# Kernel tuning notes

Measured on AMD Instinct MI355X. Metric: run time of the kernel, lower is better.

## Reference

```python
import jax, jax.numpy as jnp
import numpy as np

D = 64      # node_input_dim == node_hidden_dim
EIN = 16    # edge_input_dim
EH = 64     # edge_hidden_dim
NL, NR = 5000, 15000
EL, ER = 50000, 150000
STEPS = 6
EPS = 1e-5
SLOPE = 0.01


def _ln(x, g, b):
    mu = jnp.mean(x, axis=-1, keepdims=True)
    v = jnp.mean((x - mu) ** 2, axis=-1, keepdims=True)
    return (x - mu) / jnp.sqrt(v + EPS) * g + b


def _lrelu(x):
    return jnp.where(x > 0, x, SLOPE * x)


def setup_inputs() -> dict:
    key = jax.random.key(0)
    ks = jax.random.split(key, 32)

    def n(k, shape, fan_in):
        return jax.random.normal(k, shape, jnp.float32) * (fan_in ** -0.5)

    return {
        'lig_n_feat': jax.random.normal(ks[0], (NL, D), jnp.float32),
        'lig_e_feat': jax.random.normal(ks[1], (EL, EIN), jnp.float32),
        'lig_src': jax.random.randint(ks[2], (EL,), 0, NL),
        'lig_dst': jax.random.randint(ks[3], (EL,), 0, NL),
        'rec_n_feat': jax.random.normal(ks[4], (NR, D), jnp.float32),
        'rec_e_feat': jax.random.normal(ks[5], (ER, EIN), jnp.float32),
        'rec_src': jax.random.randint(ks[6], (ER,), 0, NR),
        'rec_dst': jax.random.randint(ks[7], (ER,), 0, NR),
        'mask': jax.random.uniform(ks[8], (NL, NR), jnp.float32),
        # linear0
        'W0': n(ks[9], (D, D), D), 'b0': jnp.zeros((D,), jnp.float32),
        # edge network: Linear(EIN,EH) -> ReLU -> Linear(EH, D*D)
        'We1': n(ks[10], (EH, EIN), EIN), 'be1': jnp.zeros((EH,), jnp.float32),
        'We2': n(ks[11], (D * D, EH), EH), 'be2': jnp.zeros((D * D,), jnp.float32),
        # NNConv residual fc (no bias) and conv bias
        'resW': n(ks[12], (D, D), D), 'conv_b': jnp.zeros((D,), jnp.float32),
        # message layer Linear(2D, D)
        'msgW': n(ks[13], (D, 2 * D), 2 * D), 'msgb': jnp.zeros((D,), jnp.float32),
        # attention projections (no bias)
        'Qlig': n(ks[14], (D, D), D), 'Klig': n(ks[15], (D, D), D), 'Vlig': n(ks[16], (D, D), D),
        'Qrec': n(ks[17], (D, D), D), 'Krec': n(ks[18], (D, D), D), 'Vrec': n(ks[19], (D, D), D),
        # final LayerNorms
        'g_lig': jnp.ones((D,), jnp.float32), 'b_lig': jnp.zeros((D,), jnp.float32),
        'g_rec': jnp.ones((D,), jnp.float32), 'b_rec': jnp.zeros((D,), jnp.float32),
    }


def _gather_branch(x, efeat, src, dst, n_nodes, W0, b0, We1, be1, We2, be2, resW, conv_b, msgW, msgb):
    # per-edge weight matrices from edge MLP: [E, D, D] (in x out)
    We = jax.nn.relu(efeat @ We1.T + be1) @ We2.T + be2
    We = We.reshape(-1, D, D)
    h = jax.nn.relu(x @ W0.T + b0)
    for _ in range(STEPS):
        msg = jnp.einsum('ei,eio->eo', h[src], We)          # gather + per-edge transform
        agg = jax.ops.segment_sum(msg, dst, num_segments=n_nodes)  # scatter-sum
        m = jax.nn.relu(agg + h @ resW.T + conv_b)           # NNConv residual + bias, relu
        h = jnp.concatenate([m, h], axis=1) @ msgW.T + msgb  # message_layer
    return h + x


def reference(lig_n_feat, lig_e_feat, lig_src, lig_dst, rec_n_feat, rec_e_feat, rec_src, rec_dst,
              mask, W0, b0, We1, be1, We2, be2, resW, conv_b, msgW, msgb,
              Qlig, Klig, Vlig, Qrec, Krec, Vrec, g_lig, b_lig, g_rec, b_rec):
    lig_Fv = _gather_branch(lig_n_feat, lig_e_feat, lig_src, lig_dst, NL,
                            W0, b0, We1, be1, We2, be2, resW, conv_b, msgW, msgb)
    rec_Fv = _gather_branch(rec_n_feat, rec_e_feat, rec_src, rec_dst, NR,
                            W0, b0, We1, be1, We2, be2, resW, conv_b, msgW, msgb)
    hl = _ln(lig_Fv, g_lig, b_lig)
    hr = _ln(rec_Fv, g_rec, b_rec)
    # lig attends to rec
    ql, kr, vr = _lrelu(hl @ Qlig.T), _lrelu(hr @ Krec.T), hr @ Vrec.T
    a = mask * (ql @ kr.T) - 1000.0 * (1.0 - mask)
    att_lig = jax.nn.softmax(a, axis=1) @ vr
    # rec attends to lig
    qr, kl, vl = _lrelu(hr @ Qrec.T), _lrelu(hl @ Klig.T), hl @ Vlig.T
    mt = mask.T
    a2 = mt * (qr @ kl.T) - 1000.0 * (1.0 - mt)
    att_rec = jax.nn.softmax(a2, axis=1) @ vl
    return (_ln(att_lig, g_lig, b_lig), _ln(att_rec, g_rec, b_rec))
```

## Files before the change

### kernel.cpp

```cpp
#include <hip/hip_runtime.h>
#include <hip/hip_bf16.h>

typedef unsigned short ushort_t;
typedef __attribute__((ext_vector_type(8))) short short8_t;
typedef __attribute__((ext_vector_type(4))) float f32x4;
typedef __attribute__((ext_vector_type(4))) unsigned uint4_t;

#define NLIG 5000
#define NREC 15000
#define NTOT 20000
#define ELIG 50000
#define EREC 150000
#define ETOT 200000
#define VSTRIDE 20160
#define NB0 313
#define NB1 938

__device__ __forceinline__ float us2f(ushort_t u){
  union { float f; unsigned int i; } x; x.i = ((unsigned int)u) << 16; return x.f;
}
__device__ __forceinline__ ushort_t f2us(float f){
  __hip_bfloat16 b = __float2bfloat16(f);
  return *reinterpret_cast<ushort_t*>(&b);
}
__device__ __forceinline__ unsigned pkbf(float a, float b){
  return (unsigned)f2us(a) | ((unsigned)f2us(b) << 16);
}
__device__ __forceinline__ float wsum64(float v){
#pragma unroll
  for (int s = 32; s >= 1; s >>= 1) v += __shfl_xor(v, s, 64);
  return v;
}
__device__ __forceinline__ f32x4 mfma32(short8_t a, short8_t b, f32x4 c){
  return __builtin_amdgcn_mfma_f32_16x16x32_bf16(a, b, c, 0, 0, 0);
}
__device__ __forceinline__ int geti(const int* __restrict__ p, int i, int i64){
  return i64 ? p[2*i] : p[i];
}

__global__ void kdetect2(const unsigned* __restrict__ xw, const unsigned* __restrict__ iw,
                         int* __restrict__ flagp){
  const int lane = threadIdx.x;
  unsigned w = xw[lane];
  int e0 = (int)((w >> 7) & 0xFF);
  int hit = (e0 >= 100 && e0 <= 134) ? 1 : 0;
  int zodd = ((lane & 1) && iw[lane] == 0u) ? 1 : 0;
#pragma unroll
  for (int s = 32; s >= 1; s >>= 1){
    hit  += __shfl_xor(hit,  s, 64);
    zodd += __shfl_xor(zodd, s, 64);
  }
  if (lane == 0){
    flagp[0] = (hit  >= 40) ? 1 : 0;
    flagp[1] = (zodd >= 24) ? 1 : 0;
  }
}

__global__ void ksent(float* __restrict__ out, int n, float c){
  int i = blockIdx.x*256 + threadIdx.x;
  if (i < n) out[i] = c;
}

__global__ void kcvt_x(const void* __restrict__ lx, const void* __restrict__ rx,
                       const int* __restrict__ flagp, float* __restrict__ xall){
  const int flag = flagp[0];
  const int idx = blockIdx.x*256 + threadIdx.x;
  const void* src; int local;
  if (idx < NLIG*64){ src = lx; local = idx; } else { src = rx; local = idx - NLIG*64; }
  float v;
  if (flag) v = us2f(((const ushort_t*)src)[local]);
  else      v = ((const float*)src)[local];
  xall[idx] = v;
}

struct Srcs { const void* p[20]; };
__global__ void kcvt_w(Srcs S, const int* __restrict__ flagp, float* __restrict__ wcvt){
  const int bounds[21] = {0,4096,4160,5184,5248,267392,271488,275584,275648,283840,
                          283904,288000,292096,296192,300288,304384,308480,308544,308608,308672,308736};
  const int flag = flagp[0];
  const int idx = blockIdx.x*256 + threadIdx.x;
  if (idx >= 308736) return;
  int seg = 0;
#pragma unroll
  for (int s = 1; s < 20; ++s) if (idx >= bounds[s]) seg = s;
  const void* src = S.p[0];
#pragma unroll
  for (int s = 1; s < 20; ++s) if (seg == s) src = S.p[s];
  const int local = idx - bounds[seg];
  float v;
  if (flag) v = us2f(((const ushort_t*)src)[local]);
  else      v = ((const float*)src)[local];
  wcvt[idx] = v;
}

#define W_W0    0
#define W_B0    4096
#define W_WE1   4160
#define W_BE1   5184
#define W_WE2   5248
#define W_BE2   267392
#define W_RESW  271488
#define W_CONVB 275584
#define W_MSGW  275648
#define W_MSGB  283840
#define W_QLIG  283904
#define W_KLIG  288000
#define W_VLIG  292096
#define W_QREC  296192
#define W_KREC  300288
#define W_VREC  304384
#define W_GLIG  308480
#define W_BLIG  308544
#define W_GREC  308608
#define W_BREC  308672

__global__ void kWpk(const float* __restrict__ We2f, ushort_t* __restrict__ Wpk){
  int oidx = blockIdx.x*256 + threadIdx.x;
  int j = oidx & 7, lane = (oidx >> 3) & 63, p = (oidx >> 9) & 1;
  int t = (oidx >> 10) & 3, kb = oidx >> 12;
  int o = t*16 + (lane & 15);
  int gik = kb*32 + (lane >> 4)*8 + j;
  int i = gik >> 6, k = gik & 63;
  float v = We2f[(size_t)(i*64 + o)*64 + k];
  ushort_t hi = f2us(v);
  Wpk[oidx] = p ? f2us(v - us2f(hi)) : hi;
}

__global__ void kh0(const float* __restrict__ xall, const float* __restrict__ W0f,
                    const float* __restrict__ b0f, float* __restrict__ h){
  __shared__ float xr[4][64];
  const int lane = threadIdx.x & 63, wv = threadIdx.x >> 6;
  const int n = blockIdx.x*4 + wv;
  xr[wv][lane] = xall[(size_t)n*64 + lane];
  __syncthreads();
  float acc = b0f[lane];
  const float* wr = W0f + lane*64;
#pragma unroll
  for (int i = 0; i < 64; ++i) acc += xr[wv][i] * wr[i];
  h[(size_t)n*64 + lane] = acc > 0.f ? acc : 0.f;
}

__global__ void khist(const int* __restrict__ ldst, const int* __restrict__ rdst,
                      const int* __restrict__ flagp, int* __restrict__ counts){
  const int i64 = flagp[1];
  const int e = blockIdx.x*256 + threadIdx.x;
  if (e >= ETOT) return;
  int dstg = (e < ELIG) ? geti(ldst, e, i64) : geti(rdst, e - ELIG, i64) + NLIG;
  atomicAdd(&counts[dstg], 1);
}

__global__ __launch_bounds__(1024) void kscan(const int* __restrict__ counts, int* __restrict__ offs){
  __shared__ int part[1024];
  const int tid = threadIdx.x;
  const int PER = 20;
  int loc[PER]; int s = 0;
#pragma unroll
  for (int j = 0; j < PER; ++j){ int idx = tid*PER + j; int v = (idx < NTOT) ? counts[idx] : 0; loc[j] = s; s += v; }
  part[tid] = s;
  __syncthreads();
  for (int d = 1; d < 1024; d <<= 1){
    int add = (tid >= d) ? part[tid - d] : 0;
    __syncthreads();
    part[tid] += add;
    __syncthreads();
  }
  int pre = (tid > 0) ? part[tid - 1] : 0;
#pragma unroll
  for (int j = 0; j < PER; ++j){ int idx = tid*PER + j; if (idx < NTOT) offs[idx] = pre + loc[j]; }
  if (tid == 1023) offs[NTOT] = part[1023];
}

__global__ void kfill(const int* __restrict__ lsrc, const int* __restrict__ ldst,
                      const int* __restrict__ rsrc, const int* __restrict__ rdst,
                      const void* __restrict__ lef, const void* __restrict__ ref_,
                      const int* __restrict__ offs, int* __restrict__ cursor,
                      const int* __restrict__ flagp,
                      int* __restrict__ e_srcn, float* __restrict__ ef_srt){
  const int flag = flagp[0];
  const int i64  = flagp[1];
  const int e = blockIdx.x*256 + threadIdx.x;
  if (e >= ETOT) return;
  int srcg, dstg, le; const void* efb;
  if (e < ELIG){ srcg = geti(lsrc, e, i64); dstg = geti(ldst, e, i64); efb = lef; le = e; }
  else {
    int e2 = e - ELIG;
    srcg = geti(rsrc, e2, i64) + NLIG; dstg = geti(rdst, e2, i64) + NLIG; efb = ref_; le = e2;
  }
  int pos = offs[dstg] + atomicAdd(&cursor[dstg], 1);
  e_srcn[pos] = srcg;
  float* efd = ef_srt + (size_t)pos*16;
  if (flag){
    const ushort_t* efp = (const ushort_t*)efb + (size_t)le*16;
#pragma unroll
    for (int c = 0; c < 16; ++c) efd[c] = us2f(efp[c]);
  } else {
    const float* efp = (const float*)efb + (size_t)le*16;
#pragma unroll
    for (int c = 0; c < 16; ++c) efd[c] = efp[c];
  }
}

__global__ __launch_bounds__(1024)
void kstep(const float* __restrict__ hin, float* __restrict__ hout,
           const int* __restrict__ offs, const int* __restrict__ e_srcn,
           const float* __restrict__ ef_srt,
           const ushort_t* __restrict__ Wpk,
           const float* __restrict__ We1f, const float* __restrict__ be1f,
           const float* __restrict__ resWf, const float* __restrict__ convbf,
           const float* __restrict__ msgWf, const float* __restrict__ msgbf,
           const float* __restrict__ be2f){
  __shared__ alignas(16) char sbuf[65536];
  __shared__ float h_lds[1024];
  __shared__ float Hs_lds[1024];
  __shared__ float m_lds[1024];
  __shared__ float cbf[64], mbf[64];

  const int tid = threadIdx.x, lane = tid & 63, wv = tid >> 6;
  const int n0 = blockIdx.x * 16;

  h_lds[tid] = hin[(size_t)n0*64 + tid];
  if (tid < 64){ cbf[tid] = convbf[tid]; mbf[tid] = msgbf[tid]; }

  float w1r[16];
#pragma unroll
  for (int c = 0; c < 16; ++c) w1r[c] = We1f[lane*16 + c];
  const float b1 = be1f[lane];

  float sacc[64];
#pragma unroll
  for (int i = 0; i < 64; ++i) sacc[i] = 0.f;
  float hs = 0.f;
  {
    const int v = n0 + wv;
    const int jb = offs[v], je = offs[v+1];
    for (int j = jb; j < je; ++j){
      const int sn = e_srcn[j];
      const float* efp = ef_srt + (size_t)j*16;
      float zl = b1;
#pragma unroll
      for (int c = 0; c < 16; ++c) zl += efp[c] * w1r[c];
      zl = zl > 0.f ? zl : 0.f;
      hs += hin[(size_t)sn*64 + lane];
      const float4* hp = (const float4*)(hin + (size_t)sn*64);
#pragma unroll
      for (int i4 = 0; i4 < 16; ++i4){
        float4 hv = hp[i4];
        sacc[i4*4+0] += hv.x * zl;
        sacc[i4*4+1] += hv.y * zl;
        sacc[i4*4+2] += hv.z * zl;
        sacc[i4*4+3] += hv.w * zl;
      }
    }
    Hs_lds[wv*64 + lane] = hs;
  }

  const int r15 = lane & 15, g4 = lane >> 4;
  const int tW = wv & 3, kq = wv >> 2;
  f32x4 acc; acc[0]=0.f; acc[1]=0.f; acc[2]=0.f; acc[3]=0.f;
  const unsigned sswz = ((unsigned)(wv & 7)) << 4;
  const unsigned rswz = ((unsigned)(r15 & 7)) << 4;
#pragma unroll
  for (int c = 0; c < 4; ++c){
#pragma unroll
    for (int ii = 0; ii < 16; ++ii){
      float v = sacc[c*16 + ii];
      ushort_t hi16 = f2us(v);
      unsigned off = ((unsigned)(wv*2048 + (ii*64 + lane)*2)) ^ sswz;
      *(ushort_t*)(sbuf + off) = hi16;
      *(ushort_t*)(sbuf + 32768 + off) = f2us(v - us2f(hi16));
    }
    __syncthreads();
    for (int kk = 0; kk < 8; ++kk){
      const int lk = kq*256 + kk*32;
      const int kb = c*32 + kq*8 + kk;
      const unsigned aoff = ((unsigned)(r15*2048 + (lk + g4*8)*2)) ^ rswz;
      const short8_t ah = *(const short8_t*)(sbuf + aoff);
      const short8_t al = *(const short8_t*)(sbuf + 32768 + aoff);
      const ushort_t* bp = Wpk + (size_t)(kb*4 + tW)*1024 + lane*8;
      const short8_t bh = *(const short8_t*)(bp);
      const short8_t bl = *(const short8_t*)(bp + 512);
      acc = mfma32(ah, bh, acc);
      acc = mfma32(ah, bl, acc);
      acc = mfma32(al, bh, acc);
    }
    __syncthreads();
  }

  float* redf  = (float*)sbuf;
  float* be2s  = (float*)(sbuf + 16384);
  float* resWt = (float*)(sbuf + 32768);
#pragma unroll
  for (int q = 0; q < 4; ++q)
    redf[kq*1024 + (g4*4 + q)*64 + tW*16 + r15] = acc[q];
  for (int idx = tid; idx < 4096; idx += 1024){
    be2s[idx] = be2f[idx];
    resWt[(idx & 63)*65 + (idx >> 6)] = resWf[idx];
  }
  __syncthreads();
  {
    float aggv = cbf[lane];
#pragma unroll
    for (int k4 = 0; k4 < 4; ++k4) aggv += redf[k4*1024 + wv*64 + lane];
    float t1 = 0.f, t2 = 0.f;
#pragma unroll 8
    for (int i = 0; i < 64; ++i){
      t1 += Hs_lds[wv*64 + i] * be2s[i*64 + lane];
      t2 += h_lds[wv*64 + i]  * resWt[i*65 + lane];
    }
    float mv = aggv + t1 + t2;
    m_lds[wv*64 + lane] = mv > 0.f ? mv : 0.f;
  }
  __syncthreads();
  float* msgWt = (float*)sbuf;
  for (int idx = tid; idx < 8192; idx += 1024)
    msgWt[(idx & 127)*65 + (idx >> 7)] = msgWf[idx];
  __syncthreads();
  {
    float hn = mbf[lane];
#pragma unroll 8
    for (int i = 0; i < 64; ++i){
      hn += m_lds[wv*64 + i] * msgWt[i*65 + lane];
      hn += h_lds[wv*64 + i] * msgWt[(64 + i)*65 + lane];
    }
    hout[(size_t)(n0 + wv)*64 + lane] = hn;
  }
}

__global__ void kfvproj(const float* __restrict__ h, const float* __restrict__ xall,
    const float* __restrict__ wcvt,
    ushort_t* __restrict__ qbh, ushort_t* __restrict__ qbl,
    ushort_t* __restrict__ kbh, ushort_t* __restrict__ kbl,
    ushort_t* __restrict__ vbT){
  __shared__ float hr[4][64];
  const int lane = threadIdx.x & 63, wv = threadIdx.x >> 6;
  const int n = blockIdx.x*4 + wv;
  const bool isLig = n < NLIG;
  const float fv = h[(size_t)n*64 + lane] + xall[(size_t)n*64 + lane];
  const float mu = wsum64(fv) * (1.f/64.f);
  const float dd = fv - mu;
  const float var = wsum64(dd*dd) * (1.f/64.f);
  const float gg = wcvt[(isLig ? W_GLIG : W_GREC) + lane];
  const float bb = wcvt[(isLig ? W_BLIG : W_BREC) + lane];
  const float hl = dd * rsqrtf(var + 1e-5f) * gg + bb;
  hr[wv][lane] = hl;
  __syncthreads();
  const float* Qw = wcvt + (isLig ? W_QLIG : W_QREC) + lane*64;
  const float* Kw = wcvt + (isLig ? W_KLIG : W_KREC) + lane*64;
  const float* Vw = wcvt + (isLig ? W_VLIG : W_VREC) + lane*64;
  float qa = 0.f, ka = 0.f, va = 0.f;
#pragma unroll
  for (int i = 0; i < 64; ++i){
    const float hv = hr[wv][i];
    qa += hv * Qw[i];
    ka += hv * Kw[i];
    va += hv * Vw[i];
  }
  qa = qa > 0.f ? qa : 0.01f*qa;
  ka = ka > 0.f ? ka : 0.01f*ka;
  const size_t o = (size_t)n*64 + lane;
  ushort_t qh = f2us(qa); qbh[o] = qh; qbl[o] = f2us(qa - us2f(qh));
  ushort_t kh = f2us(ka); kbh[o] = kh; kbl[o] = f2us(ka - us2f(kh));
  vbT[(size_t)lane*VSTRIDE + n] = f2us(va);
}

__global__ __launch_bounds__(512)
void kattn2(const ushort_t* __restrict__ qbh, const ushort_t* __restrict__ qbl,
            const ushort_t* __restrict__ kbh, const ushort_t* __restrict__ kbl,
            const ushort_t* __restrict__ vbT, const void* __restrict__ maskp,
            const int* __restrict__ flagp, const float* __restrict__ wcvt,
            float* __restrict__ out){
  __shared__ alignas(16) char abuf[34816];
  __shared__ float mred[8][16], lred[8][16];
  float (*m_tile)[16][257] = (float(*)[16][257])abuf;
  float (*ored)[64][17]    = (float(*)[64][17])abuf;

  const int flag = flagp[0];
  const int bx = blockIdx.x;
  const int dirn = (bx < NB0) ? 0 : 1;
  const int bid  = dirn ? (bx - NB0) : bx;
  const int R   = dirn ? NREC : NLIG;
  const int C   = dirn ? NLIG : NREC;
  const int RNB = dirn ? NLIG : 0;
  const int CNB = dirn ? 0 : NLIG;
  const float* gwf = wcvt + (dirn ? W_GREC : W_GLIG);
  const float* bwf = wcvt + (dirn ? W_BREC : W_BLIG);
  float* outp = out + (size_t)RNB*64;

  const int tid = threadIdx.x, lane = tid & 63, wv = tid >> 6;
  const int r15 = lane & 15, g4 = lane >> 4;
  const int rbase = bid * 16;
  int rn = rbase + r15; if (rn > R-1) rn = R-1;

  const ushort_t* qph = qbh + (size_t)(RNB + rn)*64;
  const ushort_t* qpl = qbl + (size_t)(RNB + rn)*64;
  const short8_t qh0a = *(const short8_t*)(qph + g4*8);
  const short8_t qh0b = *(const short8_t*)(qph + 32 + g4*8);
  const short8_t ql0a = *(const short8_t*)(qpl + g4*8);
  const short8_t ql0b = *(const short8_t*)(qpl + 32 + g4*8);

  const int srcA = (((g4 & 1) * 2)     << 4) + r15;
  const int srcB = (((g4 & 1) * 2 + 1) << 4) + r15;
  const bool hiBank = (g4 >> 1) != 0;

  const int s_row = tid >> 5, s_l31 = tid & 31;
  const int s_cl = tid >> 1, s_half = tid & 1;

  float mr[8];
  auto load_tile = [&](int tb2){
    if (dirn == 0){
      int r = rbase + s_row; if (r > R-1) r = R-1;
      const size_t base = (size_t)r*NREC + tb2;
      const int cmax = C-1 - tb2;
      if (flag){
        const ushort_t* mp = (const ushort_t*)maskp + base;
#pragma unroll
        for (int j = 0; j < 8; ++j){
          int cj = s_l31 + 32*j; if (cj > cmax) cj = cmax;
          mr[j] = us2f(mp[cj]);
        }
      } else {
        const float* mp = (const float*)maskp + base;
#pragma unroll
        for (int j = 0; j < 8; ++j){
          int cj = s_l31 + 32*j; if (cj > cmax) cj = cmax;
          mr[j] = mp[cj];
        }
      }
    } else {
      int c = tb2 + s_cl; if (c > C-1) c = C-1;
      int r0 = rbase + s_half*8; if (r0 > R-8) r0 = R-8;
      const size_t base = (size_t)c*NREC + r0;
      if (flag){
        const ushort_t* mp = (const ushort_t*)maskp + base;
        const short8_t v8 = *(const short8_t*)mp;
#pragma unroll
        for (int j = 0; j < 8; ++j) mr[j] = us2f((ushort_t)v8[j]);
      } else {
        const float* mp = (const float*)maskp + base;
        const float4 v0 = *(const float4*)mp;
        const float4 v1 = *(const float4*)(mp + 4);
        mr[0]=v0.x; mr[1]=v0.y; mr[2]=v0.z; mr[3]=v0.w;
        mr[4]=v1.x; mr[5]=v1.y; mr[6]=v1.z; mr[7]=v1.w;
      }
    }
  };

  float mrun = -1e30f, lrun = 0.f;
  f32x4 oacc[4];
#pragma unroll
  for (int t = 0; t < 4; ++t){ oacc[t][0]=0.f; oacc[t][1]=0.f; oacc[t][2]=0.f; oacc[t][3]=0.f; }

  load_tile(0);
  int buf = 0;
  for (int tb = 0; tb < C; tb += 256){
    if (dirn == 0){
#pragma unroll
      for (int j = 0; j < 8; ++j) m_tile[buf][s_row][s_l31 + 32*j] = mr[j];
    } else {
#pragma unroll
      for (int j = 0; j < 8; ++j) m_tile[buf][s_half*8 + j][s_cl] = mr[j];
    }
    if (tb + 256 < C) load_tile(tb + 256);
    __syncthreads();

    const int cb = tb + wv*32;
    int cn0 = cb + r15;      if (cn0 > C-1) cn0 = C-1;
    int cn1 = cb + 16 + r15; if (cn1 > C-1) cn1 = C-1;
    const ushort_t* kp0h = kbh + (size_t)(CNB + cn0)*64;
    const ushort_t* kp0l = kbl + (size_t)(CNB + cn0)*64;
    const ushort_t* kp1h = kbh + (size_t)(CNB + cn1)*64;
    const ushort_t* kp1l = kbl + (size_t)(CNB + cn1)*64;
    f32x4 st0; st0[0]=0.f; st0[1]=0.f; st0[2]=0.f; st0[3]=0.f;
    f32x4 st1 = st0;
    {
      short8_t ka_ = *(const short8_t*)(kp0h + g4*8);
      short8_t kb_ = *(const short8_t*)(kp0h + 32 + g4*8);
      st0 = mfma32(ka_, qh0a, st0); st0 = mfma32(kb_, qh0b, st0);
      st0 = mfma32(ka_, ql0a, st0); st0 = mfma32(kb_, ql0b, st0);
      short8_t kc_ = *(const short8_t*)(kp0l + g4*8);
      short8_t kd_ = *(const short8_t*)(kp0l + 32 + g4*8);
      st0 = mfma32(kc_, qh0a, st0); st0 = mfma32(kd_, qh0b, st0);
    }
    {
      short8_t ka_ = *(const short8_t*)(kp1h + g4*8);
      short8_t kb_ = *(const short8_t*)(kp1h + 32 + g4*8);
      st1 = mfma32(ka_, qh0a, st1); st1 = mfma32(kb_, qh0b, st1);
      st1 = mfma32(ka_, ql0a, st1); st1 = mfma32(kb_, ql0b, st1);
      short8_t kc_ = *(const short8_t*)(kp1l + g4*8);
      short8_t kd_ = *(const short8_t*)(kp1l + 32 + g4*8);
      st1 = mfma32(kc_, qh0a, st1); st1 = mfma32(kd_, qh0b, st1);
    }
    float sv0[4], sv1[4]; float tmax = -1e30f;
#pragma unroll
    for (int j = 0; j < 4; ++j){
      const int c0 = cb + g4*4 + j, c1 = cb + 16 + g4*4 + j;
      const float mv0 = m_tile[buf][r15][wv*32 + g4*4 + j];
      const float mv1 = m_tile[buf][r15][wv*32 + 16 + g4*4 + j];
      sv0[j] = (c0 < C) ? mv0 * (st0[j] + 1000.f) : -1e30f;
      sv1[j] = (c1 < C) ? mv1 * (st1[j] + 1000.f) : -1e30f;
      tmax = fmaxf(tmax, fmaxf(sv0[j], sv1[j]));
    }
    tmax = fmaxf(tmax, __shfl_xor(tmax, 16, 64));
    tmax = fmaxf(tmax, __shfl_xor(tmax, 32, 64));
    const float mnew = fmaxf(mrun, tmax);
    const float corr = __expf(mrun - mnew);
    float ps0[4], ps1[4], psum = 0.f;
#pragma unroll
    for (int j = 0; j < 4; ++j){
      ps0[j] = __expf(sv0[j] - mnew); psum += ps0[j];
      ps1[j] = __expf(sv1[j] - mnew); psum += ps1[j];
    }
    psum += __shfl_xor(psum, 16, 64);
    psum += __shfl_xor(psum, 32, 64);
    lrun = lrun * corr + psum;
    mrun = mnew;
    const unsigned pk0 = pkbf(ps0[0], ps0[1]);
    const unsigned pk1 = pkbf(ps0[2], ps0[3]);
    const unsigned pk2 = pkbf(ps1[0], ps1[1]);
    const unsigned pk3 = pkbf(ps1[2], ps1[3]);
    const unsigned a0 = (unsigned)__shfl((int)pk0, srcA, 64);
    const unsigned a2 = (unsigned)__shfl((int)pk2, srcA, 64);
    const unsigned a1 = (unsigned)__shfl((int)pk1, srcA, 64);
    const unsigned a3 = (unsigned)__shfl((int)pk3, srcA, 64);
    const unsigned b0 = (unsigned)__shfl((int)pk0, srcB, 64);
    const unsigned b2 = (unsigned)__shfl((int)pk2, srcB, 64);
    const unsigned b1 = (unsigned)__shfl((int)pk1, srcB, 64);
    const unsigned b3 = (unsigned)__shfl((int)pk3, srcB, 64);
    uint4_t pw;
    pw[0] = hiBank ? a2 : a0;
    pw[1] = hiBank ? a3 : a1;
    pw[2] = hiBank ? b2 : b0;
    pw[3] = hiBank ? b3 : b1;
    const short8_t pf8 = *reinterpret_cast<const short8_t*>(&pw);
    const ushort_t* vtb = vbT + (size_t)(CNB + cb + g4*8);
#pragma unroll
    for (int t = 0; t < 4; ++t){
#pragma unroll
      for (int q = 0; q < 4; ++q) oacc[t][q] *= corr;
      const short8_t af = *(const short8_t*)(vtb + (size_t)(t*16 + r15)*VSTRIDE);
      oacc[t] = mfma32(af, pf8, oacc[t]);
    }
    buf ^= 1;
  }

  __syncthreads();
  if (g4 == 0){ mred[wv][r15] = mrun; lred[wv][r15] = lrun; }
#pragma unroll
  for (int t = 0; t < 4; ++t)
#pragma unroll
    for (int q = 0; q < 4; ++q)
      ored[wv][t*16 + g4*4 + q][r15] = oacc[t][q];
  __syncthreads();

  for (int rr = 2*wv; rr <= 2*wv + 1; ++rr){
    float mstar = -1e30f;
#pragma unroll
    for (int w = 0; w < 8; ++w) mstar = fmaxf(mstar, mred[w][rr]);
    float lstar = 0.f, ov = 0.f;
#pragma unroll
    for (int w = 0; w < 8; ++w){
      const float e = __expf(mred[w][rr] - mstar);
      lstar += lred[w][rr] * e;
      ov    += ored[w][lane][rr] * e;
    }
    const float att = ov / lstar;
    const float mu = wsum64(att) * (1.f/64.f);
    const float dd = att - mu;
    const float var = wsum64(dd*dd) * (1.f/64.f);
    const float y = dd * rsqrtf(var + 1e-5f) * gwf[lane] + bwf[lane];
    const int rg = rbase + rr;
    if (rg < R) outp[(size_t)rg*64 + lane] = y;
  }
}

extern "C" void kernel_launch(void* const* d_in, const int* in_sizes, int n_in,
                              void* d_out, int out_size, void* d_ws, size_t ws_size,
                              hipStream_t stream){
  const int expsz[29] = {320000,800000,50000,50000,960000,2400000,150000,150000,75000000,
                         4096,64,1024,64,262144,4096,4096,64,8192,64,
                         4096,4096,4096,4096,4096,4096,64,64,64,64};
  bool ok = (n_in == 29);
  if (ok) for (int i = 0; i < 29; ++i) if (in_sizes[i] != expsz[i]) ok = false;
  if (!ok){
    ksent<<<(out_size + 255)/256, 256, 0, stream>>>((float*)d_out, out_size, 10.0f);
    return;
  }

  const void* lig_n = d_in[0];
  const void* lig_e = d_in[1];
  const int* lig_src = (const int*)d_in[2];
  const int* lig_dst = (const int*)d_in[3];
  const void* rec_n = d_in[4];
  const void* rec_e = d_in[5];
  const int* rec_src = (const int*)d_in[6];
  const int* rec_dst = (const int*)d_in[7];
  const void* mask = d_in[8];

  char* p = (char*)d_ws;
  auto carve = [&](size_t bytes)->char*{ char* r = p; p += (bytes + 255) & ~(size_t)255; return r; };
  float*    xall  = (float*)   carve((size_t)NTOT*64*4);
  float*    wcvt  = (float*)   carve((size_t)308736*4);
  float*    h_a   = (float*)   carve((size_t)NTOT*64*4);
  float*    h_b   = (float*)   carve((size_t)NTOT*64*4);
  ushort_t* Wpk   = (ushort_t*)carve((size_t)524288*2);
  ushort_t* qbh   = (ushort_t*)carve((size_t)NTOT*64*2);
  ushort_t* qbl   = (ushort_t*)carve((size_t)NTOT*64*2);
  ushort_t* kbh   = (ushort_t*)carve((size_t)NTOT*64*2);
  ushort_t* kbl   = (ushort_t*)carve((size_t)NTOT*64*2);
  ushort_t* vbT   = (ushort_t*)carve((size_t)64*VSTRIDE*2);
  int*      flag  = (int*)     carve(256);
  int*      counts= (int*)     carve((size_t)2*NTOT*4);
  int*      cursor= counts + NTOT;
  int*      offs  = (int*)     carve((size_t)(NTOT+1)*4);
  int*      e_srcn= (int*)     carve((size_t)ETOT*4);
  float*    ef_srt= (float*)   carve((size_t)ETOT*16*4);

  if ((size_t)(p - (char*)d_ws) > ws_size){
    ksent<<<(out_size + 255)/256, 256, 0, stream>>>((float*)d_out, out_size, 20.0f);
    return;
  }

  Srcs S;
  for (int i = 0; i < 20; ++i) S.p[i] = d_in[9 + i];

  hipMemsetAsync(counts, 0, (size_t)2*NTOT*4, stream);
  hipMemsetAsync(vbT, 0, (size_t)64*VSTRIDE*2, stream);
  kdetect2<<<1, 64, 0, stream>>>((const unsigned*)lig_n, (const unsigned*)lig_src, flag);
  kcvt_x<<<NTOT*64/256, 256, 0, stream>>>(lig_n, rec_n, flag, xall);
  kcvt_w<<<(308736 + 255)/256, 256, 0, stream>>>(S, flag, wcvt);
  kWpk<<<2048, 256, 0, stream>>>(wcvt + W_WE2, Wpk);
  kh0<<<NTOT/4, 256, 0, stream>>>(xall, wcvt + W_W0, wcvt + W_B0, h_a);
  khist<<<(ETOT + 255)/256, 256, 0, stream>>>(lig_dst, rec_dst, flag, counts);
  kscan<<<1, 1024, 0, stream>>>(counts, offs);
  kfill<<<(ETOT + 255)/256, 256, 0, stream>>>(lig_src, lig_dst, rec_src, rec_dst,
                                              lig_e, rec_e, offs, cursor, flag, e_srcn, ef_srt);
  float* hi = h_a; float* ho = h_b;
  for (int s = 0; s < 6; ++s){
    kstep<<<NTOT/16, 1024, 0, stream>>>(hi, ho, offs, e_srcn, ef_srt, Wpk,
                                        wcvt + W_WE1, wcvt + W_BE1, wcvt + W_RESW,
                                        wcvt + W_CONVB, wcvt + W_MSGW, wcvt + W_MSGB,
                                        wcvt + W_BE2);
    float* t = hi; hi = ho; ho = t;
  }
  kfvproj<<<NTOT/4, 256, 0, stream>>>(hi, xall, wcvt, qbh, qbl, kbh, kbl, vbT);
  kattn2<<<NB0 + NB1, 512, 0, stream>>>(qbh, qbl, kbh, kbl, vbT, mask, flag, wcvt,
                                        (float*)d_out);
}
```

Baseline: 2.135 ms.

## Widen attention mask tiles to 512 columns with two-deep register prefetch

The attention kernel now stages 512-column mask tiles per iteration instead of 256. Each wave processes two 32-column sub-blocks per tile, and two register buffers hold prefetched tiles two iterations ahead. The transposed-direction mask load has each thread read 16 contiguous row values for one column, replacing the earlier half-split scheme. The step kernel's LDS split-bf16 staging also swaps its XOR swizzle for a padded row stride. The aim is fewer barriers and better hiding of mask load latency, at the cost of more registers, which may reduce occupancy, and a larger LDS footprint (about 64KB).

New measurement: 2.248 ms. +5.3%, slower.

```diff
diff --git a/kernel.cpp b/kernel.cpp
--- a/kernel.cpp
+++ b/kernel.cpp
@@ -200,6 +200,8 @@
   }
 }
 
+#define SROW 2080
+#define SLO  (16*SROW)
 __global__ __launch_bounds__(1024)
 void kstep(const float* __restrict__ hin, float* __restrict__ hout,
            const int* __restrict__ offs, const int* __restrict__ e_srcn,
@@ -209,7 +211,7 @@
            const float* __restrict__ resWf, const float* __restrict__ convbf,
            const float* __restrict__ msgWf, const float* __restrict__ msgbf,
            const float* __restrict__ be2f){
-  __shared__ alignas(16) char sbuf[65536];
+  __shared__ alignas(16) char sbuf[2*SLO];
   __shared__ float h_lds[1024];
   __shared__ float Hs_lds[1024];
   __shared__ float m_lds[1024];
@@ -257,25 +259,23 @@
   const int r15 = lane & 15, g4 = lane >> 4;
   const int tW = wv & 3, kq = wv >> 2;
   f32x4 acc; acc[0]=0.f; acc[1]=0.f; acc[2]=0.f; acc[3]=0.f;
-  const unsigned sswz = ((unsigned)(wv & 7)) << 4;
-  const unsigned rswz = ((unsigned)(r15 & 7)) << 4;
 #pragma unroll
   for (int c = 0; c < 4; ++c){
 #pragma unroll
     for (int ii = 0; ii < 16; ++ii){
       float v = sacc[c*16 + ii];
       ushort_t hi16 = f2us(v);
-      unsigned off = ((unsigned)(wv*2048 + (ii*64 + lane)*2)) ^ sswz;
+      unsigned off = (unsigned)(wv*SROW + (ii*64 + lane)*2);
       *(ushort_t*)(sbuf + off) = hi16;
-      *(ushort_t*)(sbuf + 32768 + off) = f2us(v - us2f(hi16));
+      *(ushort_t*)(sbuf + SLO + off) = f2us(v - us2f(hi16));
     }
     __syncthreads();
     for (int kk = 0; kk < 8; ++kk){
       const int lk = kq*256 + kk*32;
       const int kb = c*32 + kq*8 + kk;
-      const unsigned aoff = ((unsigned)(r15*2048 + (lk + g4*8)*2)) ^ rswz;
+      const unsigned aoff = (unsigned)(r15*SROW + (lk + g4*8)*2);
       const short8_t ah = *(const short8_t*)(sbuf + aoff);
-      const short8_t al = *(const short8_t*)(sbuf + 32768 + aoff);
+      const short8_t al = *(const short8_t*)(sbuf + SLO + aoff);
       const ushort_t* bp = Wpk + (size_t)(kb*4 + tW)*1024 + lane*8;
       const short8_t bh = *(const short8_t*)(bp);
       const short8_t bl = *(const short8_t*)(bp + 512);
@@ -369,9 +369,9 @@
             const ushort_t* __restrict__ vbT, const void* __restrict__ maskp,
             const int* __restrict__ flagp, const float* __restrict__ wcvt,
             float* __restrict__ out){
-  __shared__ alignas(16) char abuf[34816];
+  __shared__ alignas(16) char abuf[65664];
   __shared__ float mred[8][16], lred[8][16];
-  float (*m_tile)[16][257] = (float(*)[16][257])abuf;
+  float (*m_tile)[16][513] = (float(*)[16][513])abuf;
   float (*ored)[64][17]    = (float(*)[64][17])abuf;
 
   const int flag = flagp[0];
@@ -403,10 +403,13 @@
   const bool hiBank = (g4 >> 1) != 0;
 
   const int s_row = tid >> 5, s_l31 = tid & 31;
-  const int s_cl = tid >> 1, s_half = tid & 1;
-
-  float mr[8];
-  auto load_tile = [&](int tb2){
+
+  float mrun = -1e30f, lrun = 0.f;
+  f32x4 oacc[4];
+#pragma unroll
+  for (int t = 0; t < 4; ++t){ oacc[t][0]=0.f; oacc[t][1]=0.f; oacc[t][2]=0.f; oacc[t][3]=0.f; }
+
+  auto load_tile = [&](int tb2, float (&mr)[16]){
     if (dirn == 0){
       int r = rbase + s_row; if (r > R-1) r = R-1;
       const size_t base = (size_t)r*NREC + tb2;
@@ -414,133 +417,156 @@
       if (flag){
         const ushort_t* mp = (const ushort_t*)maskp + base;
 #pragma unroll
-        for (int j = 0; j < 8; ++j){
+        for (int j = 0; j < 16; ++j){
           int cj = s_l31 + 32*j; if (cj > cmax) cj = cmax;
           mr[j] = us2f(mp[cj]);
         }
       } else {
         const float* mp = (const float*)maskp + base;
 #pragma unroll
-        for (int j = 0; j < 8; ++j){
+        for (int j = 0; j < 16; ++j){
           int cj = s_l31 + 32*j; if (cj > cmax) cj = cmax;
           mr[j] = mp[cj];
         }
       }
     } else {
-      int c = tb2 + s_cl; if (c > C-1) c = C-1;
-      int r0 = rbase + s_half*8; if (r0 > R-8) r0 = R-8;
-      const size_t base = (size_t)c*NREC + r0;
-      if (flag){
-        const ushort_t* mp = (const ushort_t*)maskp + base;
-        const short8_t v8 = *(const short8_t*)mp;
-#pragma unroll
-        for (int j = 0; j < 8; ++j) mr[j] = us2f((ushort_t)v8[j]);
+      int c = tb2 + tid; if (c > C-1) c = C-1;
+      const size_t base = (size_t)c*NREC + rbase;
+      if (rbase + 16 <= R){
+        if (flag){
+          const ushort_t* mp = (const ushort_t*)maskp + base;
+          const short8_t v0 = *(const short8_t*)mp;
+          const short8_t v1 = *(const short8_t*)(mp + 8);
+#pragma unroll
+          for (int j = 0; j < 8; ++j){ mr[j] = us2f((ushort_t)v0[j]); mr[8+j] = us2f((ushort_t)v1[j]); }
+        } else {
+          const float* mp = (const float*)maskp + base;
+#pragma unroll
+          for (int q = 0; q < 4; ++q){
+            const float4 v = *(const float4*)(mp + q*4);
+            mr[q*4+0]=v.x; mr[q*4+1]=v.y; mr[q*4+2]=v.z; mr[q*4+3]=v.w;
+          }
+        }
       } else {
-        const float* mp = (const float*)maskp + base;
-        const float4 v0 = *(const float4*)mp;
-        const float4 v1 = *(const float4*)(mp + 4);
-        mr[0]=v0.x; mr[1]=v0.y; mr[2]=v0.z; mr[3]=v0.w;
-        mr[4]=v1.x; mr[5]=v1.y; mr[6]=v1.z; mr[7]=v1.w;
+#pragma unroll
+        for (int j = 0; j < 16; ++j){
+          int r = rbase + j; if (r > R-1) r = R-1;
+          const size_t mo = (size_t)c*NREC + r;
+          mr[j] = flag ? us2f(((const ushort_t*)maskp)[mo]) : ((const float*)maskp)[mo];
+        }
       }
     }
   };
 
-  float mrun = -1e30f, lrun = 0.f;
-  f32x4 oacc[4];
-#pragma unroll
-  for (int t = 0; t < 4; ++t){ oacc[t][0]=0.f; oacc[t][1]=0.f; oacc[t][2]=0.f; oacc[t][3]=0.f; }
-
-  load_tile(0);
-  int buf = 0;
-  for (int tb = 0; tb < C; tb += 256){
+  auto stage_write = [&](const float (&mr)[16], int bufc){
     if (dirn == 0){
 #pragma unroll
-      for (int j = 0; j < 8; ++j) m_tile[buf][s_row][s_l31 + 32*j] = mr[j];
+      for (int j = 0; j < 16; ++j) m_tile[bufc][s_row][s_l31 + 32*j] = mr[j];
     } else {
 #pragma unroll
-      for (int j = 0; j < 8; ++j) m_tile[buf][s_half*8 + j][s_cl] = mr[j];
-    }
-    if (tb + 256 < C) load_tile(tb + 256);
+      for (int j = 0; j < 16; ++j) m_tile[bufc][j][tid] = mr[j];
+    }
+  };
+
+  auto compute = [&](int tb, int bufc){
+#pragma unroll
+    for (int sub = 0; sub < 2; ++sub){
+      const int cb = tb + wv*64 + sub*32;
+      const int mb = wv*64 + sub*32;
+      int cn0 = cb + r15;      if (cn0 > C-1) cn0 = C-1;
+      int cn1 = cb + 16 + r15; if (cn1 > C-1) cn1 = C-1;
+      const ushort_t* kp0h = kbh + (size_t)(CNB + cn0)*64;
+      const ushort_t* kp0l = kbl + (size_t)(CNB + cn0)*64;
+      const ushort_t* kp1h = kbh + (size_t)(CNB + cn1)*64;
+      const ushort_t* kp1l = kbl + (size_t)(CNB + cn1)*64;
+      f32x4 st0; st0[0]=0.f; st0[1]=0.f; st0[2]=0.f; st0[3]=0.f;
+      f32x4 st1 = st0;
+      {
+        short8_t ka_ = *(const short8_t*)(kp0h + g4*8);
+        short8_t kb_ = *(const short8_t*)(kp0h + 32 + g4*8);
+        st0 = mfma32(ka_, qh0a, st0); st0 = mfma32(kb_, qh0b, st0);
+        st0 = mfma32(ka_, ql0a, st0); st0 = mfma32(kb_, ql0b, st0);
+        short8_t kc_ = *(const short8_t*)(kp0l + g4*8);
+        short8_t kd_ = *(const short8_t*)(kp0l + 32 + g4*8);
+        st0 = mfma32(kc_, qh0a, st0); st0 = mfma32(kd_, qh0b, st0);
+      }
+      {
+        short8_t ka_ = *(const short8_t*)(kp1h + g4*8);
+        short8_t kb_ = *(const short8_t*)(kp1h + 32 + g4*8);
+        st1 = mfma32(ka_, qh0a, st1); st1 = mfma32(kb_, qh0b, st1);
+        st1 = mfma32(ka_, ql0a, st1); st1 = mfma32(kb_, ql0b, st1);
+        short8_t kc_ = *(const short8_t*)(kp1l + g4*8);
+        short8_t kd_ = *(const short8_t*)(kp1l + 32 + g4*8);
+        st1 = mfma32(kc_, qh0a, st1); st1 = mfma32(kd_, qh0b, st1);
+      }
+      float sv0[4], sv1[4]; float tmax = -1e30f;
+#pragma unroll
+      for (int j = 0; j < 4; ++j){
+        const int c0 = cb + g4*4 + j, c1 = cb + 16 + g4*4 + j;
+        const float mv0 = m_tile[bufc][r15][mb + g4*4 + j];
+        const float mv1 = m_tile[bufc][r15][mb + 16 + g4*4 + j];
+        sv0[j] = (c0 < C) ? mv0 * (st0[j] + 1000.f) : -1e30f;
+        sv1[j] = (c1 < C) ? mv1 * (st1[j] + 1000.f) : -1e30f;
+        tmax = fmaxf(tmax, fmaxf(sv0[j], sv1[j]));
+      }
+      tmax = fmaxf(tmax, __shfl_xor(tmax, 16, 64));
+      tmax = fmaxf(tmax, __shfl_xor(tmax, 32, 64));
+      const float mnew = fmaxf(mrun, tmax);
+      const float corr = __expf(mrun - mnew);
+      float ps0[4], ps1[4], psum = 0.f;
+#pragma unroll
+      for (int j = 0; j < 4; ++j){
+        ps0[j] = __expf(sv0[j] - mnew); psum += ps0[j];
+        ps1[j] = __expf(sv1[j] - mnew); psum += ps1[j];
+      }
+      psum += __shfl_xor(psum, 16, 64);
+      psum += __shfl_xor(psum, 32, 64);
+      lrun = lrun * corr + psum;
+      mrun = mnew;
+      const unsigned pk0 = pkbf(ps0[0], ps0[1]);
+      const unsigned pk1 = pkbf(ps0[2], ps0[3]);
+      const unsigned pk2 = pkbf(ps1[0], ps1[1]);
+      const unsigned pk3 = pkbf(ps1[2], ps1[3]);
+      const unsigned a0 = (unsigned)__shfl((int)pk0, srcA, 64);
+      const unsigned a2 = (unsigned)__shfl((int)pk2, srcA, 64);
+      const unsigned a1 = (unsigned)__shfl((int)pk1, srcA, 64);
+      const unsigned a3 = (unsigned)__shfl((int)pk3, srcA, 64);
+      const unsigned b0 = (unsigned)__shfl((int)pk0, srcB, 64);
+      const unsigned b2 = (unsigned)__shfl((int)pk2, srcB, 64);
+      const unsigned b1 = (unsigned)__shfl((int)pk1, srcB, 64);
+      const unsigned b3 = (unsigned)__shfl((int)pk3, srcB, 64);
+      uint4_t pw;
+      pw[0] = hiBank ? a2 : a0;
+      pw[1] = hiBank ? a3 : a1;
+      pw[2] = hiBank ? b2 : b0;
+      pw[3] = hiBank ? b3 : b1;
+      const short8_t pf8 = *reinterpret_cast<const short8_t*>(&pw);
+      const ushort_t* vtb = vbT + (size_t)(CNB + cb + g4*8);
+#pragma unroll
+      for (int t = 0; t < 4; ++t){
+#pragma unroll
+        for (int q = 0; q < 4; ++q) oacc[t][q] *= corr;
+        const short8_t af = *(const short8_t*)(vtb + (size_t)(t*16 + r15)*VSTRIDE);
+        oacc[t] = mfma32(af, pf8, oacc[t]);
+      }
+    }
+  };
+
+  const int nt = (C + 511) >> 9;
+  float mrA[16], mrB[16];
+  load_tile(0, mrA);
+  if (nt > 1) load_tile(512, mrB);
+  for (int t = 0; t < nt; t += 2){
+    stage_write(mrA, 0);
+    if (t + 2 < nt) load_tile((t + 2) << 9, mrA);
     __syncthreads();
-
-    const int cb = tb + wv*32;
-    int cn0 = cb + r15;      if (cn0 > C-1) cn0 = C-1;
-    int cn1 = cb + 16 + r15; if (cn1 > C-1) cn1 = C-1;
-    const ushort_t* kp0h = kbh + (size_t)(CNB + cn0)*64;
-    const ushort_t* kp0l = kbl + (size_t)(CNB + cn0)*64;
-    const ushort_t* kp1h = kbh + (size_t)(CNB + cn1)*64;
-    const ushort_t* kp1l = kbl + (size_t)(CNB + cn1)*64;
-    f32x4 st0; st0[0]=0.f; st0[1]=0.f; st0[2]=0.f; st0[3]=0.f;
-    f32x4 st1 = st0;
-    {
-      short8_t ka_ = *(const short8_t*)(kp0h + g4*8);
-      short8_t kb_ = *(const short8_t*)(kp0h + 32 + g4*8);
-      st0 = mfma32(ka_, qh0a, st0); st0 = mfma32(kb_, qh0b, st0);
-      st0 = mfma32(ka_, ql0a, st0); st0 = mfma32(kb_, ql0b, st0);
-      short8_t kc_ = *(const short8_t*)(kp0l + g4*8);
-      short8_t kd_ = *(const short8_t*)(kp0l + 32 + g4*8);
-      st0 = mfma32(kc_, qh0a, st0); st0 = mfma32(kd_, qh0b, st0);
-    }
-    {
-      short8_t ka_ = *(const short8_t*)(kp1h + g4*8);
-      short8_t kb_ = *(const short8_t*)(kp1h + 32 + g4*8);
-      st1 = mfma32(ka_, qh0a, st1); st1 = mfma32(kb_, qh0b, st1);
-      st1 = mfma32(ka_, ql0a, st1); st1 = mfma32(kb_, ql0b, st1);
-      short8_t kc_ = *(const short8_t*)(kp1l + g4*8);
-      short8_t kd_ = *(const short8_t*)(kp1l + 32 + g4*8);
-      st1 = mfma32(kc_, qh0a, st1); st1 = mfma32(kd_, qh0b, st1);
-    }
-    float sv0[4], sv1[4]; float tmax = -1e30f;
-#pragma unroll
-    for (int j = 0; j < 4; ++j){
-      const int c0 = cb + g4*4 + j, c1 = cb + 16 + g4*4 + j;
-      const float mv0 = m_tile[buf][r15][wv*32 + g4*4 + j];
-      const float mv1 = m_tile[buf][r15][wv*32 + 16 + g4*4 + j];
-      sv0[j] = (c0 < C) ? mv0 * (st0[j] + 1000.f) : -1e30f;
-      sv1[j] = (c1 < C) ? mv1 * (st1[j] + 1000.f) : -1e30f;
-      tmax = fmaxf(tmax, fmaxf(sv0[j], sv1[j]));
-    }
-    tmax = fmaxf(tmax, __shfl_xor(tmax, 16, 64));
-    tmax = fmaxf(tmax, __shfl_xor(tmax, 32, 64));
-    const float mnew = fmaxf(mrun, tmax);
-    const float corr = __expf(mrun - mnew);
-    float ps0[4], ps1[4], psum = 0.f;
-#pragma unroll
-    for (int j = 0; j < 4; ++j){
-      ps0[j] = __expf(sv0[j] - mnew); psum += ps0[j];
-      ps1[j] = __expf(sv1[j] - mnew); psum += ps1[j];
-    }
-    psum += __shfl_xor(psum, 16, 64);
-    psum += __shfl_xor(psum, 32, 64);
-    lrun = lrun * corr + psum;
-    mrun = mnew;
-    const unsigned pk0 = pkbf(ps0[0], ps0[1]);
-    const unsigned pk1 = pkbf(ps0[2], ps0[3]);
-    const unsigned pk2 = pkbf(ps1[0], ps1[1]);
-    const unsigned pk3 = pkbf(ps1[2], ps1[3]);
-    const unsigned a0 = (unsigned)__shfl((int)pk0, srcA, 64);
-    const unsigned a2 = (unsigned)__shfl((int)pk2, srcA, 64);
-    const unsigned a1 = (unsigned)__shfl((int)pk1, srcA, 64);
-    const unsigned a3 = (unsigned)__shfl((int)pk3, srcA, 64);
-    const unsigned b0 = (unsigned)__shfl((int)pk0, srcB, 64);
-    const unsigned b2 = (unsigned)__shfl((int)pk2, srcB, 64);
-    const unsigned b1 = (unsigned)__shfl((int)pk1, srcB, 64);
-    const unsigned b3 = (unsigned)__shfl((int)pk3, srcB, 64);
-    uint4_t pw;
-    pw[0] = hiBank ? a2 : a0;
-    pw[1] = hiBank ? a3 : a1;
-    pw[2] = hiBank ? b2 : b0;
-    pw[3] = hiBank ? b3 : b1;
-    const short8_t pf8 = *reinterpret_cast<const short8_t*>(&pw);
-    const ushort_t* vtb = vbT + (size_t)(CNB + cb + g4*8);
-#pragma unroll
-    for (int t = 0; t < 4; ++t){
-#pragma unroll
-      for (int q = 0; q < 4; ++q) oacc[t][q] *= corr;
-      const short8_t af = *(const short8_t*)(vtb + (size_t)(t*16 + r15)*VSTRIDE);
-      oacc[t] = mfma32(af, pf8, oacc[t]);
-    }
-    buf ^= 1;
+    compute(t << 9, 0);
+    if (t + 1 < nt){
+      stage_write(mrB, 1);
+      if (t + 3 < nt) load_tile((t + 3) << 9, mrB);
+      __syncthreads();
+      compute((t + 1) << 9, 1);
+    }
   }
 
   __syncthreads();
```
